# Kernel optimization log

Measured on AMD Instinct MI355X. Metric: run time of the kernel, lower is better.

## Reference

```python
import jax, jax.numpy as jnp
import numpy as np

NUM_CLASSES = 80
D_IMG = 2048
D_WORD = 300
D_MID = 1024
B = 8
CONV = 14


def setup_inputs() -> dict:
    key = jax.random.key(0)
    ks = jax.random.split(key, 6)
    s = lambda k, shape, sc: jax.random.normal(k, shape, dtype=jnp.float32) * sc
    return {
        "batch_size": B,
        "img_feature_map": jax.random.normal(ks[0], (B, D_IMG, CONV, CONV), dtype=jnp.float32),
        "word_features": jax.random.normal(ks[1], (NUM_CLASSES, D_WORD), dtype=jnp.float32),
        "W1": s(ks[2], (D_MID, D_IMG), 0.02),
        "W2": s(ks[3], (D_MID, D_WORD), 0.02),
        "W3": s(ks[4], (D_MID, D_MID), 0.02),
        "b3": jnp.zeros((D_MID,), jnp.float32),
        "Wa": s(ks[5], (1, D_MID), 0.02),
        "ba": jnp.zeros((1,), jnp.float32),
    }


def reference(batch_size, img_feature_map, word_features, W1, W2, W3, b3, Wa, ba):
    # img_feature_map: [B, D_img, H, W] -> [B, H, W, D_img] (matches torch double transpose)
    Bn, D, H, W = img_feature_map.shape
    fmap = jnp.transpose(img_feature_map, (0, 2, 3, 1))                 # [B,H,W,D]
    f_wh = jnp.einsum('bhwd,md->bhwm', fmap, W1)                        # fc_1: [B,H,W,M]
    f_wd = word_features @ W2.T                                         # fc_2: [C,M]
    # broadcast multiply (no explicit repeat) + tanh
    t = jnp.tanh(f_wh[:, :, :, None, :] * f_wd)                         # [B,H,W,C,M]
    lb = jnp.einsum('bhwcm,nm->bhwcn', t, W3) + b3                      # fc_3: [B,H,W,C,M]
    coef = jnp.einsum('bhwcm,m->bhwc', lb, Wa[0]) + ba[0]               # fc_a: [B,H,W,C]
    # softmax over spatial positions per (batch, class)
    C = coef.shape[-1]
    coef = jax.nn.softmax(coef.reshape(Bn, H * W, C), axis=1).reshape(Bn, H, W, C)
    # softmax-weighted spatial pooling -> [B, C, D]
    return jnp.einsum('bhwc,bhwd->bcd', coef, fmap)
```

## Files before the change

### kernel.cpp

```cpp
#include <hip/hip_runtime.h>
#include <hip/hip_bf16.h>
#include <stdint.h>

#define NB 8
#define DIMG 2048
#define HWN 196
#define PN 1568
#define DMID 1024
#define NC 80
#define DWORD 300
#define PART 8

typedef short bf16x8 __attribute__((ext_vector_type(8)));
typedef float f32x4 __attribute__((ext_vector_type(4)));

__device__ __forceinline__ unsigned short f2bf(float x) {
  union { float f; unsigned u; } c; c.f = x;
  unsigned r = c.u + 0x7FFFu + ((c.u >> 16) & 1u);
  return (unsigned short)(r >> 16);
}

__global__ void k_tc(const float* __restrict__ img, unsigned short* __restrict__ fmapH,
                     const float* __restrict__ W1, unsigned short* __restrict__ W1h) {
  __shared__ float tile[32][33];
  int bx = blockIdx.x;
  int tx = threadIdx.x, ty = threadIdx.y;
  if (bx < 3584) {
    int d0 = (bx & 63) * 32;
    int rem = bx >> 6;
    int h0 = (rem % 7) * 32, b = rem / 7;
    const float* src = img + (size_t)b * DIMG * HWN;
#pragma unroll
    for (int i = 0; i < 32; i += 8) {
      int hw = h0 + tx;
      tile[ty + i][tx] = (hw < HWN) ? src[(size_t)(d0 + ty + i) * HWN + hw] : 0.f;
    }
    __syncthreads();
#pragma unroll
    for (int i = 0; i < 32; i += 8) {
      int hw = h0 + ty + i;
      if (hw < HWN)
        fmapH[(size_t)(b * HWN + hw) * DIMG + d0 + tx] = f2bf(tile[tx][ty + i]);
    }
  } else {
    int tid = ty * 32 + tx;
    int i = ((bx - 3584) * 256 + tid) * 4;
    f32x4 v = *(const f32x4*)(W1 + i);
    ushort4 s;
    s.x = f2bf(v[0]); s.y = f2bf(v[1]); s.z = f2bf(v[2]); s.w = f2bf(v[3]);
    *(ushort4*)(W1h + i) = s;
  }
}

__global__ __launch_bounds__(256) void k_fwdweff(const float* __restrict__ word,
                                                 const float* __restrict__ W2,
                                                 float* __restrict__ fwd,
                                                 const float* __restrict__ Wa,
                                                 const float* __restrict__ W3,
                                                 float* __restrict__ partial) {
  __shared__ __align__(16) float w2s[64 * DWORD];
  __shared__ __align__(16) float wds[16 * DWORD];
  int bx = blockIdx.x, t = threadIdx.x;
  if (bx < 80) {
    int m0 = (bx & 15) * 64, c0 = (bx >> 4) * 16;
    const float SC = 2.8853900817779268f;
    for (int u = t; u < 64 * 75; u += 256) {
      int r = u / 75, q = u - r * 75;
      *(f32x4*)&w2s[r * DWORD + q * 4] =
          *(const f32x4*)(W2 + (size_t)(m0 + r) * DWORD + q * 4);
    }
    for (int u = t; u < 16 * 75; u += 256) {
      int r = u / 75, q = u - r * 75;
      f32x4 v = *(const f32x4*)(word + (size_t)(c0 + r) * DWORD + q * 4);
      *(f32x4*)&wds[r * DWORD + q * 4] = v * SC;
    }
    __syncthreads();
    int ci = t >> 4, mi = t & 15;
    f32x4 a0 = {0.f, 0.f, 0.f, 0.f}, a1 = a0, a2 = a0, a3 = a0;
    const float* wr = &wds[ci * DWORD];
    for (int q = 0; q < 75; ++q) {
      f32x4 wv = *(const f32x4*)&wr[q * 4];
      f32x4 b0 = *(const f32x4*)&w2s[(mi)*DWORD + q * 4];
      f32x4 b1 = *(const f32x4*)&w2s[(mi + 16) * DWORD + q * 4];
      f32x4 b2 = *(const f32x4*)&w2s[(mi + 32) * DWORD + q * 4];
      f32x4 b3 = *(const f32x4*)&w2s[(mi + 48) * DWORD + q * 4];
#pragma unroll
      for (int u = 0; u < 4; ++u) {
        a0[u] = fmaf(wv[u], b0[u], a0[u]);
        a1[u] = fmaf(wv[u], b1[u], a1[u]);
        a2[u] = fmaf(wv[u], b2[u], a2[u]);
        a3[u] = fmaf(wv[u], b3[u], a3[u]);
      }
    }
    float* dst = fwd + (size_t)(c0 + ci) * DMID + m0 + mi;
    dst[0]  = a0[0] + a0[1] + a0[2] + a0[3];
    dst[16] = a1[0] + a1[1] + a1[2] + a1[3];
    dst[32] = a2[0] + a2[1] + a2[2] + a2[3];
    dst[48] = a3[0] + a3[1] + a3[2] + a3[3];
  } else {
    int idx = bx - 80;
    int m = (idx & 3) * 256 + t;
    int n0 = (idx >> 2) * 64;
    float acc = 0.f;
    for (int n = n0; n < n0 + 64; ++n) acc = fmaf(Wa[n], W3[(size_t)n * DMID + m], acc);
    partial[(size_t)(idx >> 2) * DMID + m] = acc;
  }
}

#define GLDS(g, l) \
  __builtin_amdgcn_global_load_lds((const __attribute__((address_space(1))) void*)(g), \
                                   (__attribute__((address_space(3))) void*)(l), 16, 0, 0)

__global__ __launch_bounds__(256) void k_gemm(const unsigned short* __restrict__ A,
                                              const unsigned short* __restrict__ Bw,
                                              float* __restrict__ C) {
  __shared__ __align__(16) unsigned short As[3][64 * 64];
  __shared__ __align__(16) unsigned short Bs[3][64 * 64];
  int m0 = blockIdx.x * 64, n0 = blockIdx.y * 64;
  int koff = blockIdx.z * 1024;
  int t = threadIdx.x;
  int w = t >> 6, l = t & 63;
  int wr = w >> 1, wc = w & 1;
  f32x4 zero = {0.f, 0.f, 0.f, 0.f};
  f32x4 acc00 = zero, acc01 = zero, acc10 = zero, acc11 = zero;

  int r0 = t >> 3, c0 = t & 7;
  int r1 = r0 + 32;
  const unsigned short* ga0 = A + (size_t)(m0 + r0) * 2048 + koff + ((c0 ^ (r0 & 7)) << 3);
  const unsigned short* ga1 = A + (size_t)(m0 + r1) * 2048 + koff + ((c0 ^ (r1 & 7)) << 3);
  const unsigned short* gb0 = Bw + (size_t)(n0 + r0) * 2048 + koff + ((c0 ^ (r0 & 7)) << 3);
  const unsigned short* gb1 = Bw + (size_t)(n0 + r1) * 2048 + koff + ((c0 ^ (r1 & 7)) << 3);

  int ra = wr * 32 + (l & 15);
  int rb = wc * 32 + (l & 15);
  int cc = l >> 4;
  int a_k0 = ra * 64 + (((cc) ^ (ra & 7)) << 3);
  int a_k1 = ra * 64 + (((cc + 4) ^ (ra & 7)) << 3);
  int b_k0 = rb * 64 + (((cc) ^ (rb & 7)) << 3);
  int b_k1 = rb * 64 + (((cc + 4) ^ (rb & 7)) << 3);

#define STAGE(bi, kk) do { \
    GLDS(ga0 + (kk), &As[bi][t * 8]); \
    GLDS(ga1 + (kk), &As[bi][t * 8 + 2048]); \
    GLDS(gb0 + (kk), &Bs[bi][t * 8]); \
    GLDS(gb1 + (kk), &Bs[bi][t * 8 + 2048]); \
  } while (0)

#define COMPUTE(bi) do { \
    const unsigned short* ap = As[bi]; \
    const unsigned short* bp = Bs[bi]; \
    bf16x8 A0 = *(const bf16x8*)(ap + a_k0); \
    bf16x8 A1 = *(const bf16x8*)(ap + a_k0 + 1024); \
    bf16x8 B0 = *(const bf16x8*)(bp + b_k0); \
    bf16x8 B1 = *(const bf16x8*)(bp + b_k0 + 1024); \
    acc00 = __builtin_amdgcn_mfma_f32_16x16x32_bf16(A0, B0, acc00, 0, 0, 0); \
    acc01 = __builtin_amdgcn_mfma_f32_16x16x32_bf16(A0, B1, acc01, 0, 0, 0); \
    acc10 = __builtin_amdgcn_mfma_f32_16x16x32_bf16(A1, B0, acc10, 0, 0, 0); \
    acc11 = __builtin_amdgcn_mfma_f32_16x16x32_bf16(A1, B1, acc11, 0, 0, 0); \
    bf16x8 A2 = *(const bf16x8*)(ap + a_k1); \
    bf16x8 A3 = *(const bf16x8*)(ap + a_k1 + 1024); \
    bf16x8 B2 = *(const bf16x8*)(bp + b_k1); \
    bf16x8 B3 = *(const bf16x8*)(bp + b_k1 + 1024); \
    acc00 = __builtin_amdgcn_mfma_f32_16x16x32_bf16(A2, B2, acc00, 0, 0, 0); \
    acc01 = __builtin_amdgcn_mfma_f32_16x16x32_bf16(A2, B3, acc01, 0, 0, 0); \
    acc10 = __builtin_amdgcn_mfma_f32_16x16x32_bf16(A3, B2, acc10, 0, 0, 0); \
    acc11 = __builtin_amdgcn_mfma_f32_16x16x32_bf16(A3, B3, acc11, 0, 0, 0); \
  } while (0)

  STAGE(0, 0);
  STAGE(1, 64);
  asm volatile("s_waitcnt vmcnt(4)" ::: "memory");
  __builtin_amdgcn_s_barrier();
  __builtin_amdgcn_sched_barrier(0);
  for (int kt = 0; kt < 16; ++kt) {
    int cur = kt % 3;
    if (kt < 14) STAGE((kt + 2) % 3, (kt + 2) * 64);
    COMPUTE(cur);
    if (kt < 14) {
      asm volatile("s_waitcnt vmcnt(4)" ::: "memory");
      __builtin_amdgcn_s_barrier();
      __builtin_amdgcn_sched_barrier(0);
    } else if (kt == 14) {
      asm volatile("s_waitcnt vmcnt(0)" ::: "memory");
      __builtin_amdgcn_s_barrier();
      __builtin_amdgcn_sched_barrier(0);
    }
  }
  float* Cz = C + (size_t)blockIdx.z * (1600 * DMID);
  int cr = (l >> 4) << 2, ccn = l & 15;
#pragma unroll
  for (int q = 0; q < 4; ++q) {
    Cz[(size_t)(m0 + wr * 32 + cr + q) * DMID + n0 + wc * 32 + ccn] = acc00[q];
    Cz[(size_t)(m0 + wr * 32 + cr + q) * DMID + n0 + wc * 32 + 16 + ccn] = acc01[q];
    Cz[(size_t)(m0 + wr * 32 + 16 + cr + q) * DMID + n0 + wc * 32 + ccn] = acc10[q];
    Cz[(size_t)(m0 + wr * 32 + 16 + cr + q) * DMID + n0 + wc * 32 + 16 + ccn] = acc11[q];
  }
#undef STAGE
#undef COMPUTE
}

#define MC 64
__global__ __launch_bounds__(256) void k_coef(const float* __restrict__ fwhp,
                                              const float* __restrict__ fwd,
                                              const float* __restrict__ partial,
                                              float* __restrict__ coefp) {
  __shared__ __align__(16) float al[64][68];
  __shared__ __align__(16) float bl[16][68];
  __shared__ __align__(16) float wl[MC];
  int p0 = blockIdx.x * 64, c0 = blockIdx.y * 16, mz = blockIdx.z;
  int t = threadIdx.x;
  int pi = t >> 4, ci = t & 15;
  float acc[4];
#pragma unroll
  for (int j = 0; j < 4; ++j) acc[j] = 0.f;

  const float* fwh0 = fwhp;
  const float* fwh1 = fwhp + (size_t)1600 * DMID;

  for (int mc = 0; mc < 2; ++mc) {
    int mbase = mz * 128 + mc * MC;
    __syncthreads();
    {
      int sra = t >> 2, sca = (t & 3) << 4;
      const float* gA0 = fwh0 + (size_t)(p0 + sra) * DMID + mbase + sca;
      const float* gA1 = fwh1 + (size_t)(p0 + sra) * DMID + mbase + sca;
#pragma unroll
      for (int q = 0; q < 4; ++q) {
        f32x4 v = *(const f32x4*)&gA0[q * 4];
        f32x4 u = *(const f32x4*)&gA1[q * 4];
        *(f32x4*)&al[sra][sca + q * 4] = v + u;
      }
      int srb = t >> 4, scb = (t & 15) << 2;
      *(f32x4*)&bl[srb][scb] = *(const f32x4*)(fwd + (size_t)(c0 + srb) * DMID + mbase + scb);
      if (t < MC) {
        float v = 0.f;
#pragma unroll
        for (int s = 0; s < 16; ++s) v += partial[(size_t)s * DMID + mbase + t];
        wl[t] = -2.f * v;
      }
    }
    __syncthreads();
    for (int mm = 0; mm < MC; mm += 4) {
      f32x4 wv = *(const f32x4*)&wl[mm];
      f32x4 bv = *(const f32x4*)&bl[ci][mm];
      f32x4 av0 = *(const f32x4*)&al[pi][mm];
      f32x4 av1 = *(const f32x4*)&al[pi + 16][mm];
      f32x4 av2 = *(const f32x4*)&al[pi + 32][mm];
      f32x4 av3 = *(const f32x4*)&al[pi + 48][mm];
#pragma unroll
      for (int u = 0; u < 4; ++u) {
        float w = wv[u], b = bv[u];
        float e0 = __builtin_amdgcn_exp2f(av0[u] * b);
        float e1 = __builtin_amdgcn_exp2f(av1[u] * b);
        float e2 = __builtin_amdgcn_exp2f(av2[u] * b);
        float e3 = __builtin_amdgcn_exp2f(av3[u] * b);
        acc[0] = fmaf(w, __builtin_amdgcn_rcpf(1.f + e0), acc[0]);
        acc[1] = fmaf(w, __builtin_amdgcn_rcpf(1.f + e1), acc[1]);
        acc[2] = fmaf(w, __builtin_amdgcn_rcpf(1.f + e2), acc[2]);
        acc[3] = fmaf(w, __builtin_amdgcn_rcpf(1.f + e3), acc[3]);
      }
    }
  }
  float* cp = coefp + (size_t)mz * (PN * NC);
#pragma unroll
  for (int j = 0; j < 4; ++j) {
    int p = p0 + pi + 16 * j;
    if (p < PN) cp[(size_t)p * NC + c0 + ci] = acc[j];
  }
}

__global__ __launch_bounds__(256) void k_pool(const float* __restrict__ coefp,
                                              const float* __restrict__ img,
                                              float* __restrict__ out) {
  __shared__ __align__(16) float wt[HWN][16];
  __shared__ float red[16][16];
  __shared__ float mxs[16], inv[16];
  int dc = blockIdx.x * 256, cg = blockIdx.y * 16, b = blockIdx.z;
  int t = threadIdx.x;
  for (int i = t; i < HWN * 4; i += 256) {
    int hw = i >> 2, j4 = (i & 3) << 2;
    size_t o = (size_t)(b * HWN + hw) * NC + cg + j4;
    f32x4 s = {0.f, 0.f, 0.f, 0.f};
#pragma unroll
    for (int z = 0; z < PART; ++z) s += *(const f32x4*)&coefp[o + (size_t)z * (PN * NC)];
    *(f32x4*)&wt[hw][j4] = s;
  }
  __syncthreads();
  int j = t & 15, g = t >> 4;
  float pm = -1e30f;
  for (int hw = g; hw < HWN; hw += 16) pm = fmaxf(pm, wt[hw][j]);
  red[g][j] = pm;
  __syncthreads();
  if (t < 16) {
    float m = red[0][t];
#pragma unroll
    for (int g2 = 1; g2 < 16; ++g2) m = fmaxf(m, red[g2][t]);
    mxs[t] = m;
  }
  __syncthreads();
  float mj = mxs[j], ps = 0.f;
  for (int hw = g; hw < HWN; hw += 16) {
    float e = __builtin_amdgcn_exp2f((wt[hw][j] - mj) * 1.4426950408889634f);
    wt[hw][j] = e;
    ps += e;
  }
  red[g][j] = ps;
  __syncthreads();
  if (t < 16) {
    float s = 0.f;
#pragma unroll
    for (int g2 = 0; g2 < 16; ++g2) s += red[g2][t];
    inv[t] = 1.f / s;
  }
  __syncthreads();
  float acc[16];
#pragma unroll
  for (int q = 0; q < 16; ++q) acc[q] = 0.f;
  const float* fpd = img + ((size_t)b * DIMG + dc + t) * HWN;
  for (int hw = 0; hw < HWN; ++hw) {
    float v = fpd[hw];
#pragma unroll
    for (int q = 0; q < 16; ++q) acc[q] = fmaf(wt[hw][q], v, acc[q]);
  }
#pragma unroll
  for (int q = 0; q < 16; ++q)
    out[((size_t)b * NC + cg + q) * DIMG + dc + t] = acc[q] * inv[q];
}

extern "C" void kernel_launch(void* const* d_in, const int* in_sizes, int n_in,
                              void* d_out, int out_size, void* d_ws, size_t ws_size,
                              hipStream_t stream) {
  const float* img  = (const float*)d_in[1];
  const float* word = (const float*)d_in[2];
  const float* W1   = (const float*)d_in[3];
  const float* W2   = (const float*)d_in[4];
  const float* W3   = (const float*)d_in[5];
  const float* Wa   = (const float*)d_in[7];
  float* out = (float*)d_out;
  char* ws = (char*)d_ws;

  unsigned short* fmapH   = (unsigned short*)(ws + 0);
  unsigned short* W1h     = (unsigned short*)(ws + 6553600);
  float*          fwhp    = (float*)(ws + 10747904);
  float*          fwd     = (float*)(ws + 23855104);
  float*          partial = (float*)(ws + 24248320);
  float*          coefp   = (float*)(ws + 24313856);

  hipLaunchKernelGGL(k_tc, dim3(5632), dim3(32, 8), 0, stream, img, fmapH, W1, W1h);
  hipLaunchKernelGGL(k_fwdweff, dim3(144), dim3(256), 0, stream,
                     word, W2, fwd, Wa, W3, partial);
  hipLaunchKernelGGL(k_gemm, dim3(25, 16, 2), dim3(256), 0, stream, fmapH, W1h, fwhp);
  hipLaunchKernelGGL(k_coef, dim3(25, 5, 8), dim3(256), 0, stream, fwhp, fwd, partial, coefp);
  hipLaunchKernelGGL(k_pool, dim3(8, 5, 8), dim3(256), 0, stream, coefp, img, out);
  (void)in_sizes; (void)n_in; (void)out_size; (void)ws_size;
}
```

Before: 113.3 us.

## Merge fc_2/W_eff kernel into GEMM launch, widen transpose tiles, halve coef tiles

The separate fwd/W_eff kernel is folded into the GEMM launch as extra block ranges. Its fc_2 part is re-tiled into smaller 16x16 blocks so many more blocks run alongside the GEMM blocks. The transpose kernel now handles 64 channels per block and writes packed bf16 pairs as 32-bit stores. The coef kernel uses 32-position tiles instead of 64, doubling its grid for better occupancy. Together these remove one launch and improve parallelism, at the cost of more redundant loads of the fwd, bl and wl data across the extra blocks.

Result: faster. 103.6 us (-8.5%).

```diff
diff --git a/kernel.cpp b/kernel.cpp
--- a/kernel.cpp
+++ b/kernel.cpp
@@ -22,16 +22,16 @@
 
 __global__ void k_tc(const float* __restrict__ img, unsigned short* __restrict__ fmapH,
                      const float* __restrict__ W1, unsigned short* __restrict__ W1h) {
-  __shared__ float tile[32][33];
+  __shared__ float tile[64][33];
   int bx = blockIdx.x;
   int tx = threadIdx.x, ty = threadIdx.y;
-  if (bx < 3584) {
-    int d0 = (bx & 63) * 32;
-    int rem = bx >> 6;
+  if (bx < 1792) {
+    int d0 = (bx & 31) * 64;
+    int rem = bx >> 5;
     int h0 = (rem % 7) * 32, b = rem / 7;
     const float* src = img + (size_t)b * DIMG * HWN;
 #pragma unroll
-    for (int i = 0; i < 32; i += 8) {
+    for (int i = 0; i < 64; i += 8) {
       int hw = h0 + tx;
       tile[ty + i][tx] = (hw < HWN) ? src[(size_t)(d0 + ty + i) * HWN + hw] : 0.f;
     }
@@ -39,12 +39,17 @@
 #pragma unroll
     for (int i = 0; i < 32; i += 8) {
       int hw = h0 + ty + i;
-      if (hw < HWN)
-        fmapH[(size_t)(b * HWN + hw) * DIMG + d0 + tx] = f2bf(tile[tx][ty + i]);
+      if (hw < HWN) {
+        int d = tx * 2;
+        unsigned short lo = f2bf(tile[d][ty + i]);
+        unsigned short hi = f2bf(tile[d + 1][ty + i]);
+        unsigned v = (unsigned)lo | ((unsigned)hi << 16);
+        *(unsigned*)&fmapH[(size_t)(b * HWN + hw) * DIMG + d0 + d] = v;
+      }
     }
   } else {
     int tid = ty * 32 + tx;
-    int i = ((bx - 3584) * 256 + tid) * 4;
+    int i = ((bx - 1792) * 256 + tid) * 4;
     f32x4 v = *(const f32x4*)(W1 + i);
     ushort4 s;
     s.x = f2bf(v[0]); s.y = f2bf(v[1]); s.z = f2bf(v[2]); s.w = f2bf(v[3]);
@@ -52,103 +57,57 @@
   }
 }
 
-__global__ __launch_bounds__(256) void k_fwdweff(const float* __restrict__ word,
-                                                 const float* __restrict__ W2,
-                                                 float* __restrict__ fwd,
-                                                 const float* __restrict__ Wa,
-                                                 const float* __restrict__ W3,
-                                                 float* __restrict__ partial) {
-  __shared__ __align__(16) float w2s[64 * DWORD];
-  __shared__ __align__(16) float wds[16 * DWORD];
-  int bx = blockIdx.x, t = threadIdx.x;
-  if (bx < 80) {
-    int m0 = (bx & 15) * 64, c0 = (bx >> 4) * 16;
-    const float SC = 2.8853900817779268f;
-    for (int u = t; u < 64 * 75; u += 256) {
-      int r = u / 75, q = u - r * 75;
-      *(f32x4*)&w2s[r * DWORD + q * 4] =
-          *(const f32x4*)(W2 + (size_t)(m0 + r) * DWORD + q * 4);
-    }
-    for (int u = t; u < 16 * 75; u += 256) {
-      int r = u / 75, q = u - r * 75;
-      f32x4 v = *(const f32x4*)(word + (size_t)(c0 + r) * DWORD + q * 4);
-      *(f32x4*)&wds[r * DWORD + q * 4] = v * SC;
-    }
-    __syncthreads();
-    int ci = t >> 4, mi = t & 15;
-    f32x4 a0 = {0.f, 0.f, 0.f, 0.f}, a1 = a0, a2 = a0, a3 = a0;
-    const float* wr = &wds[ci * DWORD];
-    for (int q = 0; q < 75; ++q) {
-      f32x4 wv = *(const f32x4*)&wr[q * 4];
-      f32x4 b0 = *(const f32x4*)&w2s[(mi)*DWORD + q * 4];
-      f32x4 b1 = *(const f32x4*)&w2s[(mi + 16) * DWORD + q * 4];
-      f32x4 b2 = *(const f32x4*)&w2s[(mi + 32) * DWORD + q * 4];
-      f32x4 b3 = *(const f32x4*)&w2s[(mi + 48) * DWORD + q * 4];
-#pragma unroll
-      for (int u = 0; u < 4; ++u) {
-        a0[u] = fmaf(wv[u], b0[u], a0[u]);
-        a1[u] = fmaf(wv[u], b1[u], a1[u]);
-        a2[u] = fmaf(wv[u], b2[u], a2[u]);
-        a3[u] = fmaf(wv[u], b3[u], a3[u]);
-      }
-    }
-    float* dst = fwd + (size_t)(c0 + ci) * DMID + m0 + mi;
-    dst[0]  = a0[0] + a0[1] + a0[2] + a0[3];
-    dst[16] = a1[0] + a1[1] + a1[2] + a1[3];
-    dst[32] = a2[0] + a2[1] + a2[2] + a2[3];
-    dst[48] = a3[0] + a3[1] + a3[2] + a3[3];
-  } else {
-    int idx = bx - 80;
-    int m = (idx & 3) * 256 + t;
-    int n0 = (idx >> 2) * 64;
-    float acc = 0.f;
-    for (int n = n0; n < n0 + 64; ++n) acc = fmaf(Wa[n], W3[(size_t)n * DMID + m], acc);
-    partial[(size_t)(idx >> 2) * DMID + m] = acc;
-  }
-}
-
 #define GLDS(g, l) \
   __builtin_amdgcn_global_load_lds((const __attribute__((address_space(1))) void*)(g), \
                                    (__attribute__((address_space(3))) void*)(l), 16, 0, 0)
 
-__global__ __launch_bounds__(256) void k_gemm(const unsigned short* __restrict__ A,
-                                              const unsigned short* __restrict__ Bw,
-                                              float* __restrict__ C) {
-  __shared__ __align__(16) unsigned short As[3][64 * 64];
-  __shared__ __align__(16) unsigned short Bs[3][64 * 64];
-  int m0 = blockIdx.x * 64, n0 = blockIdx.y * 64;
-  int koff = blockIdx.z * 1024;
+__global__ __launch_bounds__(256) void k_gw(const unsigned short* __restrict__ A,
+                                            const unsigned short* __restrict__ Bw,
+                                            float* __restrict__ C,
+                                            const float* __restrict__ word,
+                                            const float* __restrict__ W2,
+                                            float* __restrict__ fwd,
+                                            const float* __restrict__ Wa,
+                                            const float* __restrict__ W3,
+                                            float* __restrict__ partial) {
+  __shared__ __align__(16) char smem[49152];
+  int bz = blockIdx.x;
   int t = threadIdx.x;
-  int w = t >> 6, l = t & 63;
-  int wr = w >> 1, wc = w & 1;
-  f32x4 zero = {0.f, 0.f, 0.f, 0.f};
-  f32x4 acc00 = zero, acc01 = zero, acc10 = zero, acc11 = zero;
-
-  int r0 = t >> 3, c0 = t & 7;
-  int r1 = r0 + 32;
-  const unsigned short* ga0 = A + (size_t)(m0 + r0) * 2048 + koff + ((c0 ^ (r0 & 7)) << 3);
-  const unsigned short* ga1 = A + (size_t)(m0 + r1) * 2048 + koff + ((c0 ^ (r1 & 7)) << 3);
-  const unsigned short* gb0 = Bw + (size_t)(n0 + r0) * 2048 + koff + ((c0 ^ (r0 & 7)) << 3);
-  const unsigned short* gb1 = Bw + (size_t)(n0 + r1) * 2048 + koff + ((c0 ^ (r1 & 7)) << 3);
-
-  int ra = wr * 32 + (l & 15);
-  int rb = wc * 32 + (l & 15);
-  int cc = l >> 4;
-  int a_k0 = ra * 64 + (((cc) ^ (ra & 7)) << 3);
-  int a_k1 = ra * 64 + (((cc + 4) ^ (ra & 7)) << 3);
-  int b_k0 = rb * 64 + (((cc) ^ (rb & 7)) << 3);
-  int b_k1 = rb * 64 + (((cc + 4) ^ (rb & 7)) << 3);
+  if (bz < 800) {
+    unsigned short* As = (unsigned short*)smem;
+    unsigned short* Bs = As + 3 * 4096;
+    int m0 = (bz % 25) * 64;
+    int n0 = ((bz / 25) & 15) * 64;
+    int koff = (bz / 400) * 1024;
+    int w = t >> 6, l = t & 63;
+    int wr = w >> 1, wc = w & 1;
+    f32x4 zero = {0.f, 0.f, 0.f, 0.f};
+    f32x4 acc00 = zero, acc01 = zero, acc10 = zero, acc11 = zero;
+
+    int r0 = t >> 3, c0 = t & 7;
+    int r1 = r0 + 32;
+    const unsigned short* ga0 = A + (size_t)(m0 + r0) * 2048 + koff + ((c0 ^ (r0 & 7)) << 3);
+    const unsigned short* ga1 = A + (size_t)(m0 + r1) * 2048 + koff + ((c0 ^ (r1 & 7)) << 3);
+    const unsigned short* gb0 = Bw + (size_t)(n0 + r0) * 2048 + koff + ((c0 ^ (r0 & 7)) << 3);
+    const unsigned short* gb1 = Bw + (size_t)(n0 + r1) * 2048 + koff + ((c0 ^ (r1 & 7)) << 3);
+
+    int ra = wr * 32 + (l & 15);
+    int rb = wc * 32 + (l & 15);
+    int cc = l >> 4;
+    int a_k0 = ra * 64 + (((cc) ^ (ra & 7)) << 3);
+    int a_k1 = ra * 64 + (((cc + 4) ^ (ra & 7)) << 3);
+    int b_k0 = rb * 64 + (((cc) ^ (rb & 7)) << 3);
+    int b_k1 = rb * 64 + (((cc + 4) ^ (rb & 7)) << 3);
 
 #define STAGE(bi, kk) do { \
-    GLDS(ga0 + (kk), &As[bi][t * 8]); \
-    GLDS(ga1 + (kk), &As[bi][t * 8 + 2048]); \
-    GLDS(gb0 + (kk), &Bs[bi][t * 8]); \
-    GLDS(gb1 + (kk), &Bs[bi][t * 8 + 2048]); \
+    GLDS(ga0 + (kk), As + (bi) * 4096 + t * 8); \
+    GLDS(ga1 + (kk), As + (bi) * 4096 + t * 8 + 2048); \
+    GLDS(gb0 + (kk), Bs + (bi) * 4096 + t * 8); \
+    GLDS(gb1 + (kk), Bs + (bi) * 4096 + t * 8 + 2048); \
   } while (0)
-
 #define COMPUTE(bi) do { \
-    const unsigned short* ap = As[bi]; \
-    const unsigned short* bp = Bs[bi]; \
+    const unsigned short* ap = As + (bi) * 4096; \
+    const unsigned short* bp = Bs + (bi) * 4096; \
     bf16x8 A0 = *(const bf16x8*)(ap + a_k0); \
     bf16x8 A1 = *(const bf16x8*)(ap + a_k0 + 1024); \
     bf16x8 B0 = *(const bf16x8*)(bp + b_k0); \
@@ -167,36 +126,68 @@
     acc11 = __builtin_amdgcn_mfma_f32_16x16x32_bf16(A3, B3, acc11, 0, 0, 0); \
   } while (0)
 
-  STAGE(0, 0);
-  STAGE(1, 64);
-  asm volatile("s_waitcnt vmcnt(4)" ::: "memory");
-  __builtin_amdgcn_s_barrier();
-  __builtin_amdgcn_sched_barrier(0);
-  for (int kt = 0; kt < 16; ++kt) {
-    int cur = kt % 3;
-    if (kt < 14) STAGE((kt + 2) % 3, (kt + 2) * 64);
-    COMPUTE(cur);
-    if (kt < 14) {
-      asm volatile("s_waitcnt vmcnt(4)" ::: "memory");
-      __builtin_amdgcn_s_barrier();
-      __builtin_amdgcn_sched_barrier(0);
-    } else if (kt == 14) {
-      asm volatile("s_waitcnt vmcnt(0)" ::: "memory");
-      __builtin_amdgcn_s_barrier();
-      __builtin_amdgcn_sched_barrier(0);
-    }
-  }
-  float* Cz = C + (size_t)blockIdx.z * (1600 * DMID);
-  int cr = (l >> 4) << 2, ccn = l & 15;
-#pragma unroll
-  for (int q = 0; q < 4; ++q) {
-    Cz[(size_t)(m0 + wr * 32 + cr + q) * DMID + n0 + wc * 32 + ccn] = acc00[q];
-    Cz[(size_t)(m0 + wr * 32 + cr + q) * DMID + n0 + wc * 32 + 16 + ccn] = acc01[q];
-    Cz[(size_t)(m0 + wr * 32 + 16 + cr + q) * DMID + n0 + wc * 32 + ccn] = acc10[q];
-    Cz[(size_t)(m0 + wr * 32 + 16 + cr + q) * DMID + n0 + wc * 32 + 16 + ccn] = acc11[q];
-  }
+    STAGE(0, 0);
+    STAGE(1, 64);
+    asm volatile("s_waitcnt vmcnt(4)" ::: "memory");
+    __builtin_amdgcn_s_barrier();
+    __builtin_amdgcn_sched_barrier(0);
+    for (int kt = 0; kt < 16; ++kt) {
+      int cur = kt % 3;
+      if (kt < 14) STAGE((kt + 2) % 3, (kt + 2) * 64);
+      COMPUTE(cur);
+      if (kt < 14) {
+        asm volatile("s_waitcnt vmcnt(4)" ::: "memory");
+        __builtin_amdgcn_s_barrier();
+        __builtin_amdgcn_sched_barrier(0);
+      } else if (kt == 14) {
+        asm volatile("s_waitcnt vmcnt(0)" ::: "memory");
+        __builtin_amdgcn_s_barrier();
+        __builtin_amdgcn_sched_barrier(0);
+      }
+    }
+    float* Cz = C + (size_t)(bz / 400) * (1600 * DMID);
+    int cr = (l >> 4) << 2, ccn = l & 15;
+#pragma unroll
+    for (int q = 0; q < 4; ++q) {
+      Cz[(size_t)(m0 + wr * 32 + cr + q) * DMID + n0 + wc * 32 + ccn] = acc00[q];
+      Cz[(size_t)(m0 + wr * 32 + cr + q) * DMID + n0 + wc * 32 + 16 + ccn] = acc01[q];
+      Cz[(size_t)(m0 + wr * 32 + 16 + cr + q) * DMID + n0 + wc * 32 + ccn] = acc10[q];
+      Cz[(size_t)(m0 + wr * 32 + 16 + cr + q) * DMID + n0 + wc * 32 + 16 + ccn] = acc11[q];
+    }
 #undef STAGE
 #undef COMPUTE
+  } else if (bz < 1120) {
+    float* w2s = (float*)smem;
+    float* wds = w2s + 16 * 300;
+    int idx = bz - 800;
+    int m0 = (idx & 63) * 16, c0 = (idx >> 6) * 16;
+    const float SC = 2.8853900817779268f;
+    for (int u = t; u < 16 * 75; u += 256) {
+      int r = u / 75, q = u - r * 75;
+      *(f32x4*)&w2s[r * 300 + q * 4] = *(const f32x4*)(W2 + (size_t)(m0 + r) * DWORD + q * 4);
+      f32x4 v = *(const f32x4*)(word + (size_t)(c0 + r) * DWORD + q * 4);
+      *(f32x4*)&wds[r * 300 + q * 4] = v * SC;
+    }
+    __syncthreads();
+    int ci = t >> 4, mi = t & 15;
+    f32x4 av = {0.f, 0.f, 0.f, 0.f};
+    const float* wr_ = &wds[ci * 300];
+    const float* w2r = &w2s[mi * 300];
+    for (int q = 0; q < 75; ++q) {
+      f32x4 wv = *(const f32x4*)&wr_[q * 4];
+      f32x4 bv = *(const f32x4*)&w2r[q * 4];
+#pragma unroll
+      for (int u = 0; u < 4; ++u) av[u] = fmaf(wv[u], bv[u], av[u]);
+    }
+    fwd[(size_t)(c0 + ci) * DMID + m0 + mi] = av[0] + av[1] + av[2] + av[3];
+  } else {
+    int idx = bz - 1120;
+    int m = (idx & 3) * 256 + t;
+    int n0 = (idx >> 2) * 64;
+    float acc = 0.f;
+    for (int n = n0; n < n0 + 64; ++n) acc = fmaf(Wa[n], W3[(size_t)n * DMID + m], acc);
+    partial[(size_t)(idx >> 2) * DMID + m] = acc;
+  }
 }
 
 #define MC 64
@@ -204,16 +195,13 @@
                                               const float* __restrict__ fwd,
                                               const float* __restrict__ partial,
                                               float* __restrict__ coefp) {
-  __shared__ __align__(16) float al[64][68];
+  __shared__ __align__(16) float al[32][68];
   __shared__ __align__(16) float bl[16][68];
   __shared__ __align__(16) float wl[MC];
-  int p0 = blockIdx.x * 64, c0 = blockIdx.y * 16, mz = blockIdx.z;
+  int p0 = blockIdx.x * 32, c0 = blockIdx.y * 16, mz = blockIdx.z;
   int t = threadIdx.x;
   int pi = t >> 4, ci = t & 15;
-  float acc[4];
-#pragma unroll
-  for (int j = 0; j < 4; ++j) acc[j] = 0.f;
-
+  float acc[2] = {0.f, 0.f};
   const float* fwh0 = fwhp;
   const float* fwh1 = fwhp + (size_t)1600 * DMID;
 
@@ -221,11 +209,11 @@
     int mbase = mz * 128 + mc * MC;
     __syncthreads();
     {
-      int sra = t >> 2, sca = (t & 3) << 4;
+      int sra = t >> 3, sca = (t & 7) << 3;
       const float* gA0 = fwh0 + (size_t)(p0 + sra) * DMID + mbase + sca;
       const float* gA1 = fwh1 + (size_t)(p0 + sra) * DMID + mbase + sca;
 #pragma unroll
-      for (int q = 0; q < 4; ++q) {
+      for (int q = 0; q < 2; ++q) {
         f32x4 v = *(const f32x4*)&gA0[q * 4];
         f32x4 u = *(const f32x4*)&gA1[q * 4];
         *(f32x4*)&al[sra][sca + q * 4] = v + u;
@@ -245,25 +233,19 @@
       f32x4 bv = *(const f32x4*)&bl[ci][mm];
       f32x4 av0 = *(const f32x4*)&al[pi][mm];
       f32x4 av1 = *(const f32x4*)&al[pi + 16][mm];
-      f32x4 av2 = *(const f32x4*)&al[pi + 32][mm];
-      f32x4 av3 = *(const f32x4*)&al[pi + 48][mm];
 #pragma unroll
       for (int u = 0; u < 4; ++u) {
         float w = wv[u], b = bv[u];
         float e0 = __builtin_amdgcn_exp2f(av0[u] * b);
         float e1 = __builtin_amdgcn_exp2f(av1[u] * b);
-        float e2 = __builtin_amdgcn_exp2f(av2[u] * b);
-        float e3 = __builtin_amdgcn_exp2f(av3[u] * b);
         acc[0] = fmaf(w, __builtin_amdgcn_rcpf(1.f + e0), acc[0]);
         acc[1] = fmaf(w, __builtin_amdgcn_rcpf(1.f + e1), acc[1]);
-        acc[2] = fmaf(w, __builtin_amdgcn_rcpf(1.f + e2), acc[2]);
-        acc[3] = fmaf(w, __builtin_amdgcn_rcpf(1.f + e3), acc[3]);
       }
     }
   }
   float* cp = coefp + (size_t)mz * (PN * NC);
 #pragma unroll
-  for (int j = 0; j < 4; ++j) {
+  for (int j = 0; j < 2; ++j) {
     int p = p0 + pi + 16 * j;
     if (p < PN) cp[(size_t)p * NC + c0 + ci] = acc[j];
   }
@@ -346,11 +328,10 @@
   float*          partial = (float*)(ws + 24248320);
   float*          coefp   = (float*)(ws + 24313856);
 
-  hipLaunchKernelGGL(k_tc, dim3(5632), dim3(32, 8), 0, stream, img, fmapH, W1, W1h);
-  hipLaunchKernelGGL(k_fwdweff, dim3(144), dim3(256), 0, stream,
-                     word, W2, fwd, Wa, W3, partial);
-  hipLaunchKernelGGL(k_gemm, dim3(25, 16, 2), dim3(256), 0, stream, fmapH, W1h, fwhp);
-  hipLaunchKernelGGL(k_coef, dim3(25, 5, 8), dim3(256), 0, stream, fwhp, fwd, partial, coefp);
+  hipLaunchKernelGGL(k_tc, dim3(3840), dim3(32, 8), 0, stream, img, fmapH, W1, W1h);
+  hipLaunchKernelGGL(k_gw, dim3(1184), dim3(256), 0, stream,
+                     fmapH, W1h, fwhp, word, W2, fwd, Wa, W3, partial);
+  hipLaunchKernelGGL(k_coef, dim3(49, 5, 8), dim3(256), 0, stream, fwhp, fwd, partial, coefp);
   hipLaunchKernelGGL(k_pool, dim3(8, 5, 8), dim3(256), 0, stream, coefp, img, out);
   (void)in_sizes; (void)n_in; (void)out_size; (void)ws_size;
 }
```
